# Kernel tuning notes

Measured on AMD Instinct MI355X. Metric: run time of the kernel, lower is better.

## Reference

```python
import jax, jax.numpy as jnp
import numpy as np

N, E, DIM, EDIM, H, T = 30000, 300000, 64, 16, 3, 6


def setup_inputs() -> dict:
    key = jax.random.key(0)
    ks = jax.random.split(key, 20)
    s = 0.1
    inp = {
        'x': jax.random.normal(ks[0], (N, DIM), jnp.float32),
        'edge_index': jax.random.randint(ks[1], (2, E), 0, N, jnp.int64),
        'edge_attr': jax.random.normal(ks[2], (E, EDIM), jnp.float32),
        # EdgeGATConv params (heads=3, out per head = DIM, concat=False -> head mean)
        'Wg': jax.random.normal(ks[3], (DIM, H * DIM), jnp.float32) * s,
        'bg': jnp.zeros((DIM,), jnp.float32),
        'a_src': jax.random.normal(ks[4], (H, DIM), jnp.float32) * s,
        'a_dst': jax.random.normal(ks[5], (H, DIM), jnp.float32) * s,
        'We': jax.random.normal(ks[6], (EDIM, H * DIM), jnp.float32) * s,
        'a_edge': jax.random.normal(ks[7], (H, DIM), jnp.float32) * s,
        # GRU (1 layer), torch gate order: r, z, n
        'Wih': jax.random.normal(ks[8], (3 * DIM, DIM), jnp.float32) * s,
        'Whh': jax.random.normal(ks[9], (3 * DIM, DIM), jnp.float32) * s,
        'bih': jnp.zeros((3 * DIM,), jnp.float32),
        'bhh': jnp.zeros((3 * DIM,), jnp.float32),
        # NodeLevelBatchNorm per time step
        'gamma': jnp.ones((T, DIM), jnp.float32),
        'beta': jnp.zeros((T, DIM), jnp.float32),
        # final linear: dim*(T+1) -> dim
        'Wlin': jax.random.normal(ks[10], (DIM * (T + 1), DIM), jnp.float32) * s,
        'blin': jnp.zeros((DIM,), jnp.float32),
    }
    return inp


def _edge_gat(x, edge_index, edge_attr, Wg, bg, a_src, a_dst, We, a_edge):
    n = x.shape[0]
    xw = (x @ Wg).reshape(n, H, DIM)                 # [N,H,C]
    ew = (edge_attr @ We).reshape(-1, H, DIM)        # [E,H,C]
    src, dst = edge_index[0], edge_index[1]
    logits = ((xw[src] * a_src).sum(-1)
              + (xw[dst] * a_dst).sum(-1)
              + (ew * a_edge).sum(-1))               # [E,H]
    logits = jax.nn.leaky_relu(logits, 0.2)
    # segment softmax over incoming edges per destination node
    amax = jax.ops.segment_max(logits, dst, num_segments=n)
    amax = jnp.where(jnp.isfinite(amax), amax, 0.0)
    ex = jnp.exp(logits - amax[dst])
    denom = jax.ops.segment_sum(ex, dst, num_segments=n)
    att = ex / (denom[dst] + 1e-16)                  # [E,H]
    agg = jax.ops.segment_sum(xw[src] * att[..., None], dst, num_segments=n)  # [N,H,C]
    return agg.mean(axis=1) + bg                     # concat=False: head mean


def _gru_step(m, h, Wih, Whh, bih, bhh):
    gi = m @ Wih.T + bih
    gh = h @ Whh.T + bhh
    ir, iz, inn = jnp.split(gi, 3, axis=-1)
    hr, hz, hn = jnp.split(gh, 3, axis=-1)
    r = jax.nn.sigmoid(ir + hr)
    z = jax.nn.sigmoid(iz + hz)
    nn_ = jnp.tanh(inn + r * hn)
    return (1.0 - z) * nn_ + z * h


def _node_bn(x, gamma, beta, eps=1e-5):
    mu = x.mean(axis=0)
    var = ((x - mu) ** 2).mean(axis=0)
    return (x - mu) * jax.lax.rsqrt(var + eps) * gamma + beta


def reference(x, edge_index, edge_attr, Wg, bg, a_src, a_dst, We, a_edge,
              Wih, Whh, bih, bhh, gamma, beta, Wlin, blin):
    h = x
    feats = [x]
    for i in range(T):
        m = jax.nn.celu(_edge_gat(x, edge_index, edge_attr, Wg, bg, a_src, a_dst, We, a_edge))
        h = _gru_step(m, h, Wih, Whh, bih, bhh)
        x = _node_bn(h, gamma[i], beta[i])
        feats.append(x)
    return jnp.concatenate(feats, axis=-1) @ Wlin + blin
```

## Files before the change

kernel.cpp:

```cpp
#include <hip/hip_runtime.h>
#include <math.h>

constexpr int N_ = 30000;
constexpr int E_ = 300000;
constexpr int SCB = (N_ + 255) / 256;
constexpr int GB_ = (N_ + 63) / 64;

using f32x4  = __attribute__((ext_vector_type(4))) float;
using bf16x8 = __attribute__((ext_vector_type(8))) short;

__device__ __forceinline__ float4 ldg4(const float* p){ return *reinterpret_cast<const float4*>(p); }

__device__ __forceinline__ unsigned short f2bf(float f){
  union { float f; unsigned int u; } v; v.f = f;
  unsigned int r = v.u + 0x7FFFu + ((v.u >> 16) & 1u);
  return (unsigned short)(r >> 16);
}
__device__ __forceinline__ float bf2f(unsigned short b){
  union { unsigned int u; float f; } v; v.u = ((unsigned int)b) << 16;
  return v.f;
}
__device__ __forceinline__ float sigmoidf_(float x){ return 1.0f/(1.0f + __expf(-x)); }


__global__ void k_wfrag(const float* __restrict__ Wg, const float* __restrict__ Wih,
                        const float* __restrict__ Whh, const float* __restrict__ Wlin,
                        const float* __restrict__ We, const float* __restrict__ a_edge,
                        unsigned short* __restrict__ fG, unsigned short* __restrict__ fI,
                        unsigned short* __restrict__ fH, unsigned short* __restrict__ fL,
                        float* __restrict__ P, int* __restrict__ deg){
  if (blockIdx.x >= 257){
    int i = (blockIdx.x - 257)*256 + threadIdx.x;
    if (i < N_) deg[i] = 0;
    return;
  }
  if (blockIdx.x == 256){
    int t = threadIdx.x; if (t >= 48) return;
    int j = t / 3, h = t % 3;
    float s = 0.f;
    for (int c = 0; c < 64; ++c) s += We[j*192 + h*64 + c] * a_edge[h*64 + c];
    P[j*3 + h] = s;
    return;
  }
  int id = blockIdx.x*256 + threadIdx.x;
  int lid, KT;
  unsigned short* dst; int mode;
  if (id < 12288)      { lid = id;         KT = 2;  dst = fG; mode = 0; }
  else if (id < 24576) { lid = id - 12288; KT = 2;  dst = fI; mode = 1; }
  else if (id < 36864) { lid = id - 24576; KT = 2;  dst = fH; mode = 2; }
  else                 { lid = id - 36864; KT = 14; dst = fL; mode = 3; }
  int j = lid & 7, l = (lid >> 3) & 63, rest = lid >> 9;
  int kt = rest % KT, nt = rest / KT;
  int k = kt*32 + (l>>4)*8 + j;
  int n = nt*16 + (l&15);
  float v;
  if (mode == 0)      v = Wg[k*192 + n];
  else if (mode == 1) v = Wih[n*64 + k];
  else if (mode == 2) v = Whh[n*64 + k];
  else                v = Wlin[k*64 + n];
  dst[lid] = f2bf(v);
}

__global__ void k_hist(const int* __restrict__ ei, int* __restrict__ deg){
  int e = blockIdx.x*256 + threadIdx.x;
  if (e < E_) atomicAdd(&deg[ei[E_ + e]], 1);
}

__global__ void k_scanA(const int* __restrict__ deg, int* __restrict__ partial){
  int i = blockIdx.x*256 + threadIdx.x;
  int v = (i < N_) ? deg[i] : 0;
  #pragma unroll
  for (int off = 1; off < 64; off <<= 1) v += __shfl_xor(v, off);
  __shared__ int ws[4];
  if ((threadIdx.x & 63) == 0) ws[threadIdx.x >> 6] = v;
  __syncthreads();
  if (threadIdx.x == 0) partial[blockIdx.x] = ws[0] + ws[1] + ws[2] + ws[3];
}

__global__ void k_scanB(int* __restrict__ partial, int* __restrict__ row_ptr){
  __shared__ int s[128];
  int t = threadIdx.x;
  int v = (t < SCB) ? partial[t] : 0;
  s[t] = v; __syncthreads();
  for (int off = 1; off < 128; off <<= 1){
    int u = (t >= off) ? s[t-off] : 0;
    __syncthreads();
    s[t] += u;
    __syncthreads();
  }
  if (t < SCB) partial[t] = s[t] - v;
  if (t == 0) row_ptr[N_] = E_;
}

__global__ void k_scanC(const int* __restrict__ deg, const int* __restrict__ partial,
                        int* __restrict__ row_ptr, int* __restrict__ cursor){
  __shared__ int s[256];
  int t = threadIdx.x, i = blockIdx.x*256 + t;
  int v = (i < N_) ? deg[i] : 0;
  s[t] = v; __syncthreads();
  for (int off = 1; off < 256; off <<= 1){
    int u = (t >= off) ? s[t-off] : 0;
    __syncthreads();
    s[t] += u;
    __syncthreads();
  }
  int ex = s[t] - v + partial[blockIdx.x];
  if (i < N_){ row_ptr[i] = ex; cursor[i] = ex; }
}

__global__ void k_scatter(const int* __restrict__ ei, const float* __restrict__ edge_attr,
                          const float* __restrict__ P,
                          int* __restrict__ cursor, int* __restrict__ src_s,
                          int* __restrict__ dst_s, float* __restrict__ el_s){
  __shared__ float sP[48];
  int t = threadIdx.x;
  if (t < 48) sP[t] = P[t];
  __syncthreads();
  int e = blockIdx.x*256 + t;
  if (e >= E_) return;
  const float* ea = edge_attr + (size_t)e*16;
  float v[16];
  #pragma unroll
  for (int q = 0; q < 4; ++q){
    float4 f = ldg4(ea + q*4);
    v[q*4+0]=f.x; v[q*4+1]=f.y; v[q*4+2]=f.z; v[q*4+3]=f.w;
  }
  float l0=0.f,l1=0.f,l2=0.f;
  #pragma unroll
  for (int j = 0; j < 16; ++j){
    l0 += v[j]*sP[j*3+0]; l1 += v[j]*sP[j*3+1]; l2 += v[j]*sP[j*3+2];
  }
  int d = ei[E_ + e];
  int p = atomicAdd(&cursor[d], 1);
  src_s[p] = ei[e];
  dst_s[p] = d;
  el_s[p*3+0] = l0; el_s[p*3+1] = l1; el_s[p*3+2] = l2;
}


__global__ __launch_bounds__(256) void k_xw(
    const float* __restrict__ hsrc,
    const float* __restrict__ bn_stats,
    const float* __restrict__ gamma, const float* __restrict__ beta,
    int gidx, int bn,
    const unsigned short* __restrict__ fG,
    const float* __restrict__ a_src, const float* __restrict__ a_dst,
    unsigned short* __restrict__ xw,
    float* __restrict__ asrc, float* __restrict__ adst,
    unsigned short* __restrict__ fr)
{
  __shared__ short sAf[8*64*8];
  __shared__ unsigned short sXW[64*196];
  __shared__ float sSc[64], sSh[64];
  const int t = threadIdx.x;
  const int row0 = blockIdx.x * 64;
  if (t < 64){
    float sc = 1.f, sh = 0.f;
    if (bn){
      float mu  = bn_stats[t] * (1.0f/30000.0f);
      float var = bn_stats[64+t] * (1.0f/30000.0f) - mu*mu;
      float rs = rsqrtf(var + 1e-5f);
      sc = gamma[gidx*64 + t] * rs;
      sh = beta[gidx*64 + t] - mu*sc;
    }
    sSc[t] = sc; sSh[t] = sh;
  }
  __syncthreads();
  {
    const int lr = t >> 4, k4 = (t & 15) * 4;
    const float sc0=sSc[k4],sc1=sSc[k4+1],sc2=sSc[k4+2],sc3=sSc[k4+3];
    const float sh0=sSh[k4],sh1=sSh[k4+1],sh2=sSh[k4+2],sh3=sSh[k4+3];
    const int kt = k4 >> 5, lanew = lr + (((k4>>3)&3)<<4), j0 = k4 & 7;
    #pragma unroll
    for (int i = 0; i < 4; ++i){
      int r = lr + i*16, gr = row0 + r;
      float4 v = make_float4(0.f,0.f,0.f,0.f);
      if (gr < N_){
        v = ldg4(hsrc + (size_t)gr*64 + k4);
        v.x = fmaf(v.x, sc0, sh0); v.y = fmaf(v.y, sc1, sh1);
        v.z = fmaf(v.z, sc2, sh2); v.w = fmaf(v.w, sc3, sh3);
      }
      ushort4 pk; pk.x=f2bf(v.x); pk.y=f2bf(v.y); pk.z=f2bf(v.z); pk.w=f2bf(v.w);
      *reinterpret_cast<ushort4*>(&sAf[((i*2+kt)*64 + lanew)*8 + j0]) = pk;
    }
  }
  __syncthreads();
  {
    bf16x8 v0 = *reinterpret_cast<bf16x8*>(&sAf[t*8]);
    bf16x8 v1 = *reinterpret_cast<bf16x8*>(&sAf[2048 + t*8]);
    bf16x8* g = reinterpret_cast<bf16x8*>(fr + (size_t)blockIdx.x*4096);
    g[t] = v0; g[256 + t] = v1;
  }
  const int w = t >> 6, l = t & 63, q = l >> 4, b = l & 15;
  f32x4 acc[12];
  #pragma unroll
  for (int nt = 0; nt < 12; ++nt) acc[nt] = (f32x4){0.f,0.f,0.f,0.f};
  bf16x8 a0 = *reinterpret_cast<bf16x8*>(&sAf[((w*2+0)*64 + l)*8]);
  bf16x8 a1 = *reinterpret_cast<bf16x8*>(&sAf[((w*2+1)*64 + l)*8]);
  #pragma unroll
  for (int nt = 0; nt < 12; ++nt){
    bf16x8 b0 = *reinterpret_cast<const bf16x8*>(fG + (size_t)((nt*2+0)*64 + l)*8);
    bf16x8 b1 = *reinterpret_cast<const bf16x8*>(fG + (size_t)((nt*2+1)*64 + l)*8);
    acc[nt] = __builtin_amdgcn_mfma_f32_16x16x32_bf16(a0, b0, acc[nt], 0, 0, 0);
    acc[nt] = __builtin_amdgcn_mfma_f32_16x16x32_bf16(a1, b1, acc[nt], 0, 0, 0);
  }
  float asl[3][4], adl[3][4];
  #pragma unroll
  for (int h = 0; h < 3; ++h)
    #pragma unroll
    for (int u = 0; u < 4; ++u){
      asl[h][u] = a_src[h*64 + u*16 + b];
      adl[h][u] = a_dst[h*64 + u*16 + b];
    }
  #pragma unroll
  for (int r = 0; r < 4; ++r){
    int gr = row0 + w*16 + q*4 + r;
    #pragma unroll
    for (int h = 0; h < 3; ++h){
      float s = 0.f, d = 0.f;
      #pragma unroll
      for (int u = 0; u < 4; ++u){
        s = fmaf(acc[4*h+u][r], asl[h][u], s);
        d = fmaf(acc[4*h+u][r], adl[h][u], d);
      }
      s += __shfl_xor(s,1); s += __shfl_xor(s,2); s += __shfl_xor(s,4); s += __shfl_xor(s,8);
      d += __shfl_xor(d,1); d += __shfl_xor(d,2); d += __shfl_xor(d,4); d += __shfl_xor(d,8);
      if (b == h && gr < N_){ asrc[gr*3+h] = s; adst[gr*3+h] = d; }
    }
  }
  #pragma unroll
  for (int nt = 0; nt < 12; ++nt){
    int col = nt*16 + b;
    #pragma unroll
    for (int r = 0; r < 4; ++r)
      sXW[(w*16 + q*4 + r)*196 + col] = f2bf(acc[nt][r]);
  }
  __syncthreads();
  #pragma unroll
  for (int i = 0; i < 16; ++i){
    int id = i*256 + t;
    int row = id >> 6, c2 = id & 63, gr = row0 + row;
    if (gr < N_){
      ushort4 pv;
      pv.x = sXW[row*196 + c2];
      pv.y = sXW[row*196 + 64 + c2];
      pv.z = sXW[row*196 + 128 + c2];
      pv.w = 0;
      *reinterpret_cast<ushort4*>(xw + ((size_t)gr << 8) + (c2 << 2)) = pv;
    }
  }
}

__global__ void k_att(const int* __restrict__ src_s, const int* __restrict__ dst_s,
                      const float* __restrict__ el_s,
                      const float* __restrict__ asrc, const float* __restrict__ adst,
                      float* __restrict__ att_s){
  int p = blockIdx.x*256 + threadIdx.x;
  if (p >= E_) return;
  int s = src_s[p], d = dst_s[p];
  #pragma unroll
  for (int h = 0; h < 3; ++h){
    float l = asrc[s*3+h] + adst[d*3+h] + el_s[p*3+h];
    l = l > 0.f ? l : 0.2f*l;
    att_s[p*3+h] = __expf(l);
  }
}

__global__ __launch_bounds__(256) void k_agg(
    const int* __restrict__ row_ptr, const int* __restrict__ src_s,
    const float* __restrict__ att_s,
    const unsigned short* __restrict__ xw,
    const float* __restrict__ bg,
    float* __restrict__ mbuf, float* __restrict__ bn_stats)
{
  if (blockIdx.x == 0 && threadIdx.x < 128) bn_stats[threadIdx.x] = 0.f;
  int n = blockIdx.x*4 + (threadIdx.x >> 6);
  int c = threadIdx.x & 63;
  if (n >= N_) return;
  int p0 = row_ptr[n], p1 = row_ptr[n+1];
  float d0 = 0.f, d1 = 0.f, d2 = 0.f;
  float a0 = 0.f, a1 = 0.f, a2 = 0.f;
  int p = p0;
  for (; p + 4 <= p1; p += 4){
    int sA = src_s[p], sB = src_s[p+1], sC = src_s[p+2], sD = src_s[p+3];
    ushort4 gA = *reinterpret_cast<const ushort4*>(xw + ((size_t)sA << 8) + (c << 2));
    ushort4 gB = *reinterpret_cast<const ushort4*>(xw + ((size_t)sB << 8) + (c << 2));
    ushort4 gC = *reinterpret_cast<const ushort4*>(xw + ((size_t)sC << 8) + (c << 2));
    ushort4 gD = *reinterpret_cast<const ushort4*>(xw + ((size_t)sD << 8) + (c << 2));
    float wA0 = att_s[p*3+0],  wA1 = att_s[p*3+1],  wA2 = att_s[p*3+2];
    float wB0 = att_s[p*3+3],  wB1 = att_s[p*3+4],  wB2 = att_s[p*3+5];
    float wC0 = att_s[p*3+6],  wC1 = att_s[p*3+7],  wC2 = att_s[p*3+8];
    float wD0 = att_s[p*3+9],  wD1 = att_s[p*3+10], wD2 = att_s[p*3+11];
    d0 += (wA0 + wB0) + (wC0 + wD0);
    d1 += (wA1 + wB1) + (wC1 + wD1);
    d2 += (wA2 + wB2) + (wC2 + wD2);
    a0 = fmaf(wA0, bf2f(gA.x), a0); a1 = fmaf(wA1, bf2f(gA.y), a1); a2 = fmaf(wA2, bf2f(gA.z), a2);
    a0 = fmaf(wB0, bf2f(gB.x), a0); a1 = fmaf(wB1, bf2f(gB.y), a1); a2 = fmaf(wB2, bf2f(gB.z), a2);
    a0 = fmaf(wC0, bf2f(gC.x), a0); a1 = fmaf(wC1, bf2f(gC.y), a1); a2 = fmaf(wC2, bf2f(gC.z), a2);
    a0 = fmaf(wD0, bf2f(gD.x), a0); a1 = fmaf(wD1, bf2f(gD.y), a1); a2 = fmaf(wD2, bf2f(gD.z), a2);
  }
  for (; p < p1; ++p){
    int s = src_s[p];
    ushort4 g = *reinterpret_cast<const ushort4*>(xw + ((size_t)s << 8) + (c << 2));
    float w0 = att_s[p*3+0], w1 = att_s[p*3+1], w2 = att_s[p*3+2];
    d0 += w0; d1 += w1; d2 += w2;
    a0 = fmaf(w0, bf2f(g.x), a0);
    a1 = fmaf(w1, bf2f(g.y), a1);
    a2 = fmaf(w2, bf2f(g.z), a2);
  }
  float mp = (a0/(d0+1e-16f) + a1/(d1+1e-16f) + a2/(d2+1e-16f)) * (1.0f/3.0f) + bg[c];
  mbuf[(size_t)n*64 + c] = mp > 0.f ? mp : (__expf(mp) - 1.0f);
}

__global__ __launch_bounds__(256) void k_gru(
    const float* __restrict__ mbuf, const float* __restrict__ hsrc,
    float* __restrict__ hbuf,
    const unsigned short* __restrict__ fI, const unsigned short* __restrict__ fH,
    const float* __restrict__ bih, const float* __restrict__ bhh,
    float* __restrict__ bn_stats)
{
  __shared__ short sMf[8*64*8];
  __shared__ short sHf[8*64*8];
  __shared__ float sH[64][68];
  __shared__ float sStat[128];
  const int t = threadIdx.x;
  const int row0 = blockIdx.x * 64;
  if (t < 128) sStat[t] = 0.f;
  {
    const int lr = t >> 4, k4 = (t & 15) * 4;
    const int kt = k4 >> 5, lanew = lr + (((k4>>3)&3)<<4), j0 = k4 & 7;
    #pragma unroll
    for (int i = 0; i < 4; ++i){
      int r = lr + i*16, gr = row0 + r;
      float4 vm = make_float4(0.f,0.f,0.f,0.f), vh = vm;
      if (gr < N_){ vm = ldg4(mbuf + (size_t)gr*64 + k4); vh = ldg4(hsrc + (size_t)gr*64 + k4); }
      ushort4 pm; pm.x=f2bf(vm.x); pm.y=f2bf(vm.y); pm.z=f2bf(vm.z); pm.w=f2bf(vm.w);
      ushort4 ph; ph.x=f2bf(vh.x); ph.y=f2bf(vh.y); ph.z=f2bf(vh.z); ph.w=f2bf(vh.w);
      *reinterpret_cast<ushort4*>(&sMf[((i*2+kt)*64 + lanew)*8 + j0]) = pm;
      *reinterpret_cast<ushort4*>(&sHf[((i*2+kt)*64 + lanew)*8 + j0]) = ph;
      sH[r][k4+0]=vh.x; sH[r][k4+1]=vh.y; sH[r][k4+2]=vh.z; sH[r][k4+3]=vh.w;
    }
  }
  __syncthreads();
  const int w = t >> 6, l = t & 63, q = l >> 4, b = l & 15;
  f32x4 aI[12], aH[12];
  #pragma unroll
  for (int nt = 0; nt < 12; ++nt){ aI[nt] = (f32x4){0.f,0.f,0.f,0.f}; aH[nt] = (f32x4){0.f,0.f,0.f,0.f}; }
  bf16x8 am0 = *reinterpret_cast<bf16x8*>(&sMf[((w*2+0)*64 + l)*8]);
  bf16x8 am1 = *reinterpret_cast<bf16x8*>(&sMf[((w*2+1)*64 + l)*8]);
  bf16x8 ah0 = *reinterpret_cast<bf16x8*>(&sHf[((w*2+0)*64 + l)*8]);
  bf16x8 ah1 = *reinterpret_cast<bf16x8*>(&sHf[((w*2+1)*64 + l)*8]);
  #pragma unroll
  for (int nt = 0; nt < 12; ++nt){
    bf16x8 bI0 = *reinterpret_cast<const bf16x8*>(fI + (size_t)((nt*2+0)*64 + l)*8);
    bf16x8 bI1 = *reinterpret_cast<const bf16x8*>(fI + (size_t)((nt*2+1)*64 + l)*8);
    bf16x8 bH0 = *reinterpret_cast<const bf16x8*>(fH + (size_t)((nt*2+0)*64 + l)*8);
    bf16x8 bH1 = *reinterpret_cast<const bf16x8*>(fH + (size_t)((nt*2+1)*64 + l)*8);
    aI[nt] = __builtin_amdgcn_mfma_f32_16x16x32_bf16(am0, bI0, aI[nt], 0, 0, 0);
    aI[nt] = __builtin_amdgcn_mfma_f32_16x16x32_bf16(am1, bI1, aI[nt], 0, 0, 0);
    aH[nt] = __builtin_amdgcn_mfma_f32_16x16x32_bf16(ah0, bH0, aH[nt], 0, 0, 0);
    aH[nt] = __builtin_amdgcn_mfma_f32_16x16x32_bf16(ah1, bH1, aH[nt], 0, 0, 0);
  }
  float s1[4] = {0.f,0.f,0.f,0.f}, s2[4] = {0.f,0.f,0.f,0.f};
  #pragma unroll
  for (int tt = 0; tt < 4; ++tt){
    int c = tt*16 + b;
    float bir = bih[c], biz = bih[64+c], bin = bih[128+c];
    float bhr = bhh[c], bhz = bhh[64+c], bhn = bhh[128+c];
    #pragma unroll
    for (int r = 0; r < 4; ++r){
      int row = w*16 + q*4 + r, gr = row0 + row;
      float rg = sigmoidf_(aI[tt][r]   + bir + aH[tt][r]   + bhr);
      float zg = sigmoidf_(aI[tt+4][r] + biz + aH[tt+4][r] + bhz);
      float ng = tanhf(aI[tt+8][r] + bin + rg*(aH[tt+8][r] + bhn));
      float ho = sH[row][c];
      float hv = (1.f - zg)*ng + zg*ho;
      if (gr < N_){
        hbuf[(size_t)gr*64 + c] = hv;
        s1[tt] += hv; s2[tt] += hv*hv;
      }
    }
  }
  #pragma unroll
  for (int tt = 0; tt < 4; ++tt){
    float v = s1[tt];
    v += __shfl_xor(v, 16); v += __shfl_xor(v, 32);
    float u = s2[tt];
    u += __shfl_xor(u, 16); u += __shfl_xor(u, 32);
    if (q == 0){
      atomicAdd(&sStat[tt*16 + b], v);
      atomicAdd(&sStat[64 + tt*16 + b], u);
    }
  }
  __syncthreads();
  if (t < 128) atomicAdd(&bn_stats[t], sStat[t]);
}

__global__ __launch_bounds__(256) void k_final(
    const unsigned short* __restrict__ ff, const float* __restrict__ hbuf,
    const float* __restrict__ bn_stats,
    const float* __restrict__ gamma, const float* __restrict__ beta,
    const unsigned short* __restrict__ fL, const float* __restrict__ blin,
    float* __restrict__ out)
{
  __shared__ short sAf[8*64*8];
  __shared__ float sSc[64], sSh[64];
  const int t = threadIdx.x;
  const int row0 = blockIdx.x * 64;
  if (t < 64){
    float mu  = bn_stats[t] * (1.0f/30000.0f);
    float var = bn_stats[64+t] * (1.0f/30000.0f) - mu*mu;
    float rs = rsqrtf(var + 1e-5f);
    float sc = gamma[5*64 + t] * rs;
    sSc[t] = sc;
    sSh[t] = beta[5*64 + t] - mu*sc;
  }
  __syncthreads();
  const int w = t >> 6, l = t & 63, q = l >> 4, b = l & 15;
  const int lr = t >> 4, k4 = (t & 15) * 4;
  const int kt = k4 >> 5, lanew = lr + (((k4>>3)&3)<<4), j0 = k4 & 7;
  {
    #pragma unroll
    for (int i = 0; i < 4; ++i){
      int r = lr + i*16, gr = row0 + r;
      float4 v = make_float4(0.f,0.f,0.f,0.f);
      if (gr < N_){
        v = ldg4(hbuf + (size_t)gr*64 + k4);
        v.x = fmaf(v.x, sSc[k4+0], sSh[k4+0]);
        v.y = fmaf(v.y, sSc[k4+1], sSh[k4+1]);
        v.z = fmaf(v.z, sSc[k4+2], sSh[k4+2]);
        v.w = fmaf(v.w, sSc[k4+3], sSh[k4+3]);
      }
      ushort4 pk; pk.x=f2bf(v.x); pk.y=f2bf(v.y); pk.z=f2bf(v.z); pk.w=f2bf(v.w);
      *reinterpret_cast<ushort4*>(&sAf[((i*2+kt)*64 + lanew)*8 + j0]) = pk;
    }
  }
  __syncthreads();
  f32x4 acc[4];
  #pragma unroll
  for (int nt = 0; nt < 4; ++nt) acc[nt] = (f32x4){0.f,0.f,0.f,0.f};
  const unsigned short* fb = ff + (size_t)blockIdx.x*4096;
  #pragma unroll
  for (int kc = 0; kc < 6; ++kc){
    const unsigned short* fs = fb + (size_t)kc*GB_*4096;
    bf16x8 a0 = *reinterpret_cast<const bf16x8*>(fs + (w*2+0)*512 + l*8);
    bf16x8 a1 = *reinterpret_cast<const bf16x8*>(fs + (w*2+1)*512 + l*8);
    #pragma unroll
    for (int nt = 0; nt < 4; ++nt){
      bf16x8 b0 = *reinterpret_cast<const bf16x8*>(fL + (size_t)((nt*14 + kc*2+0)*64 + l)*8);
      bf16x8 b1 = *reinterpret_cast<const bf16x8*>(fL + (size_t)((nt*14 + kc*2+1)*64 + l)*8);
      acc[nt] = __builtin_amdgcn_mfma_f32_16x16x32_bf16(a0, b0, acc[nt], 0, 0, 0);
      acc[nt] = __builtin_amdgcn_mfma_f32_16x16x32_bf16(a1, b1, acc[nt], 0, 0, 0);
    }
  }
  {
    bf16x8 a0 = *reinterpret_cast<bf16x8*>(&sAf[((w*2+0)*64 + l)*8]);
    bf16x8 a1 = *reinterpret_cast<bf16x8*>(&sAf[((w*2+1)*64 + l)*8]);
    #pragma unroll
    for (int nt = 0; nt < 4; ++nt){
      bf16x8 b0 = *reinterpret_cast<const bf16x8*>(fL + (size_t)((nt*14 + 12)*64 + l)*8);
      bf16x8 b1 = *reinterpret_cast<const bf16x8*>(fL + (size_t)((nt*14 + 13)*64 + l)*8);
      acc[nt] = __builtin_amdgcn_mfma_f32_16x16x32_bf16(a0, b0, acc[nt], 0, 0, 0);
      acc[nt] = __builtin_amdgcn_mfma_f32_16x16x32_bf16(a1, b1, acc[nt], 0, 0, 0);
    }
  }
  #pragma unroll
  for (int nt = 0; nt < 4; ++nt){
    int col = nt*16 + b;
    float bl = blin[col];
    #pragma unroll
    for (int r = 0; r < 4; ++r){
      int gr = row0 + w*16 + q*4 + r;
      if (gr < N_) out[(size_t)gr*64 + col] = acc[nt][r] + bl;
    }
  }
}


extern "C" void kernel_launch(void* const* d_in, const int* in_sizes, int n_in,
                              void* d_out, int out_size, void* d_ws, size_t ws_size,
                              hipStream_t stream) {
  const float* x        = (const float*)d_in[0];
  const int*   ei       = (const int*)  d_in[1];
  const float* edge_attr= (const float*)d_in[2];
  const float* Wg       = (const float*)d_in[3];
  const float* bg       = (const float*)d_in[4];
  const float* a_src    = (const float*)d_in[5];
  const float* a_dst    = (const float*)d_in[6];
  const float* We       = (const float*)d_in[7];
  const float* a_edge   = (const float*)d_in[8];
  const float* Wih      = (const float*)d_in[9];
  const float* Whh      = (const float*)d_in[10];
  const float* bih      = (const float*)d_in[11];
  const float* bhh      = (const float*)d_in[12];
  const float* gamma    = (const float*)d_in[13];
  const float* beta     = (const float*)d_in[14];
  const float* Wlin     = (const float*)d_in[15];
  const float* blin     = (const float*)d_in[16];
  float* out = (float*)d_out;

  char* w = (char*)d_ws;
  auto alloc = [&](size_t bytes) -> void* {
    void* p = (void*)w;
    w += (bytes + 255) & ~(size_t)255;
    return p;
  };
  int*   row_ptr = (int*)  alloc((size_t)(N_+1)*4);
  int*   deg     = (int*)  alloc((size_t)N_*4);
  int*   cursor  = (int*)  alloc((size_t)N_*4);
  int*   partial = (int*)  alloc(128*4);
  int*   src_s   = (int*)  alloc((size_t)E_*4);
  int*   dst_s   = (int*)  alloc((size_t)E_*4);
  float* el_s    = (float*)alloc((size_t)E_*3*4);
  float* att_s   = (float*)alloc((size_t)E_*3*4);
  float* Pw      = (float*)alloc(48*4);
  unsigned short* fG = (unsigned short*)alloc(12288*2);
  unsigned short* fI = (unsigned short*)alloc(12288*2);
  unsigned short* fH = (unsigned short*)alloc(12288*2);
  unsigned short* fL = (unsigned short*)alloc(28672*2);
  unsigned short* xw = (unsigned short*)alloc((size_t)N_*256*2);
  unsigned short* ffrag = (unsigned short*)alloc((size_t)6*GB_*4096*2);
  float* asrc    = (float*)alloc((size_t)N_*3*4);
  float* adst    = (float*)alloc((size_t)N_*3*4);
  float* mbuf    = (float*)alloc((size_t)N_*64*4);
  float* hbuf    = (float*)alloc((size_t)N_*64*4);
  float* bn_stats= (float*)alloc(128*4);

  const int EB = (E_ + 255)/256;

  k_wfrag  <<<257 + SCB, 256, 0, stream>>>(Wg, Wih, Whh, Wlin, We, a_edge,
                                           fG, fI, fH, fL, Pw, deg);
  k_hist   <<<EB, 256, 0, stream>>>(ei, deg);
  k_scanA  <<<SCB, 256, 0, stream>>>(deg, partial);
  k_scanB  <<<1, 128, 0, stream>>>(partial, row_ptr);
  k_scanC  <<<SCB, 256, 0, stream>>>(deg, partial, row_ptr, cursor);
  k_scatter<<<EB, 256, 0, stream>>>(ei, edge_attr, Pw, cursor, src_s, dst_s, el_s);

  for (int step = 0; step < 6; ++step){
    const float* hsrc = (step == 0) ? x : hbuf;
    k_xw <<<GB_, 256, 0, stream>>>(hsrc, bn_stats, gamma, beta,
                                   step-1, step > 0 ? 1 : 0,
                                   fG, a_src, a_dst, xw, asrc, adst,
                                   ffrag + (size_t)step*GB_*4096);
    k_att<<<EB, 256, 0, stream>>>(src_s, dst_s, el_s, asrc, adst, att_s);
    k_agg<<<(N_+3)/4, 256, 0, stream>>>(row_ptr, src_s, att_s, xw, bg, mbuf, bn_stats);
    k_gru<<<GB_, 256, 0, stream>>>(mbuf, hsrc, hbuf, fI, fH, bih, bhh, bn_stats);
  }
  k_final<<<GB_, 256, 0, stream>>>(ffrag, hbuf, bn_stats, gamma, beta, fL, blin, out);
}
```

Measured before the change: 559.0 us.

## Fuse attention, aggregation and GRU into one kernel per step

Removes the separate attention and aggregation kernels. Edge logits are now recomputed inside the aggregation loop, and the aggregated message is written straight into the GRU's shared-memory bf16 fragments instead of a global mbuf. The dst_s, att_s and mbuf buffers go away, and BN stats become per-step slices zeroed once at setup. The cost is that aggregation now runs at 64-row-block granularity with one wave per row sequentially, which lowers parallelism for the gather phase, and the unroll drops from 4 to 2.

```diff
diff --git a/kernel.cpp b/kernel.cpp
--- a/kernel.cpp
+++ b/kernel.cpp
@@ -28,7 +28,12 @@
                         const float* __restrict__ We, const float* __restrict__ a_edge,
                         unsigned short* __restrict__ fG, unsigned short* __restrict__ fI,
                         unsigned short* __restrict__ fH, unsigned short* __restrict__ fL,
-                        float* __restrict__ P, int* __restrict__ deg){
+                        float* __restrict__ P, int* __restrict__ deg,
+                        float* __restrict__ bn_stats){
+  if (blockIdx.x == 257 + SCB){
+    for (int k = threadIdx.x; k < 768; k += 256) bn_stats[k] = 0.f;
+    return;
+  }
   if (blockIdx.x >= 257){
     int i = (blockIdx.x - 257)*256 + threadIdx.x;
     if (i < N_) deg[i] = 0;
@@ -111,7 +116,7 @@
 __global__ void k_scatter(const int* __restrict__ ei, const float* __restrict__ edge_attr,
                           const float* __restrict__ P,
                           int* __restrict__ cursor, int* __restrict__ src_s,
-                          int* __restrict__ dst_s, float* __restrict__ el_s){
+                          float* __restrict__ el_s){
   __shared__ float sP[48];
   int t = threadIdx.x;
   if (t < 48) sP[t] = P[t];
@@ -133,7 +138,6 @@
   int d = ei[E_ + e];
   int p = atomicAdd(&cursor[d], 1);
   src_s[p] = ei[e];
-  dst_s[p] = d;
   el_s[p*3+0] = l0; el_s[p*3+1] = l1; el_s[p*3+2] = l2;
 }
 
@@ -251,70 +255,12 @@
   }
 }
 
-__global__ void k_att(const int* __restrict__ src_s, const int* __restrict__ dst_s,
-                      const float* __restrict__ el_s,
-                      const float* __restrict__ asrc, const float* __restrict__ adst,
-                      float* __restrict__ att_s){
-  int p = blockIdx.x*256 + threadIdx.x;
-  if (p >= E_) return;
-  int s = src_s[p], d = dst_s[p];
-  #pragma unroll
-  for (int h = 0; h < 3; ++h){
-    float l = asrc[s*3+h] + adst[d*3+h] + el_s[p*3+h];
-    l = l > 0.f ? l : 0.2f*l;
-    att_s[p*3+h] = __expf(l);
-  }
-}
-
-__global__ __launch_bounds__(256) void k_agg(
+__global__ __launch_bounds__(256) void k_aggru(
     const int* __restrict__ row_ptr, const int* __restrict__ src_s,
-    const float* __restrict__ att_s,
-    const unsigned short* __restrict__ xw,
-    const float* __restrict__ bg,
-    float* __restrict__ mbuf, float* __restrict__ bn_stats)
-{
-  if (blockIdx.x == 0 && threadIdx.x < 128) bn_stats[threadIdx.x] = 0.f;
-  int n = blockIdx.x*4 + (threadIdx.x >> 6);
-  int c = threadIdx.x & 63;
-  if (n >= N_) return;
-  int p0 = row_ptr[n], p1 = row_ptr[n+1];
-  float d0 = 0.f, d1 = 0.f, d2 = 0.f;
-  float a0 = 0.f, a1 = 0.f, a2 = 0.f;
-  int p = p0;
-  for (; p + 4 <= p1; p += 4){
-    int sA = src_s[p], sB = src_s[p+1], sC = src_s[p+2], sD = src_s[p+3];
-    ushort4 gA = *reinterpret_cast<const ushort4*>(xw + ((size_t)sA << 8) + (c << 2));
-    ushort4 gB = *reinterpret_cast<const ushort4*>(xw + ((size_t)sB << 8) + (c << 2));
-    ushort4 gC = *reinterpret_cast<const ushort4*>(xw + ((size_t)sC << 8) + (c << 2));
-    ushort4 gD = *reinterpret_cast<const ushort4*>(xw + ((size_t)sD << 8) + (c << 2));
-    float wA0 = att_s[p*3+0],  wA1 = att_s[p*3+1],  wA2 = att_s[p*3+2];
-    float wB0 = att_s[p*3+3],  wB1 = att_s[p*3+4],  wB2 = att_s[p*3+5];
-    float wC0 = att_s[p*3+6],  wC1 = att_s[p*3+7],  wC2 = att_s[p*3+8];
-    float wD0 = att_s[p*3+9],  wD1 = att_s[p*3+10], wD2 = att_s[p*3+11];
-    d0 += (wA0 + wB0) + (wC0 + wD0);
-    d1 += (wA1 + wB1) + (wC1 + wD1);
-    d2 += (wA2 + wB2) + (wC2 + wD2);
-    a0 = fmaf(wA0, bf2f(gA.x), a0); a1 = fmaf(wA1, bf2f(gA.y), a1); a2 = fmaf(wA2, bf2f(gA.z), a2);
-    a0 = fmaf(wB0, bf2f(gB.x), a0); a1 = fmaf(wB1, bf2f(gB.y), a1); a2 = fmaf(wB2, bf2f(gB.z), a2);
-    a0 = fmaf(wC0, bf2f(gC.x), a0); a1 = fmaf(wC1, bf2f(gC.y), a1); a2 = fmaf(wC2, bf2f(gC.z), a2);
-    a0 = fmaf(wD0, bf2f(gD.x), a0); a1 = fmaf(wD1, bf2f(gD.y), a1); a2 = fmaf(wD2, bf2f(gD.z), a2);
-  }
-  for (; p < p1; ++p){
-    int s = src_s[p];
-    ushort4 g = *reinterpret_cast<const ushort4*>(xw + ((size_t)s << 8) + (c << 2));
-    float w0 = att_s[p*3+0], w1 = att_s[p*3+1], w2 = att_s[p*3+2];
-    d0 += w0; d1 += w1; d2 += w2;
-    a0 = fmaf(w0, bf2f(g.x), a0);
-    a1 = fmaf(w1, bf2f(g.y), a1);
-    a2 = fmaf(w2, bf2f(g.z), a2);
-  }
-  float mp = (a0/(d0+1e-16f) + a1/(d1+1e-16f) + a2/(d2+1e-16f)) * (1.0f/3.0f) + bg[c];
-  mbuf[(size_t)n*64 + c] = mp > 0.f ? mp : (__expf(mp) - 1.0f);
-}
-
-__global__ __launch_bounds__(256) void k_gru(
-    const float* __restrict__ mbuf, const float* __restrict__ hsrc,
-    float* __restrict__ hbuf,
+    const float* __restrict__ el_s,
+    const float* __restrict__ asrc, const float* __restrict__ adst,
+    const unsigned short* __restrict__ xw, const float* __restrict__ bg,
+    const float* __restrict__ hsrc, float* __restrict__ hbuf,
     const unsigned short* __restrict__ fI, const unsigned short* __restrict__ fH,
     const float* __restrict__ bih, const float* __restrict__ bhh,
     float* __restrict__ bn_stats)
@@ -332,17 +278,62 @@
     #pragma unroll
     for (int i = 0; i < 4; ++i){
       int r = lr + i*16, gr = row0 + r;
-      float4 vm = make_float4(0.f,0.f,0.f,0.f), vh = vm;
-      if (gr < N_){ vm = ldg4(mbuf + (size_t)gr*64 + k4); vh = ldg4(hsrc + (size_t)gr*64 + k4); }
-      ushort4 pm; pm.x=f2bf(vm.x); pm.y=f2bf(vm.y); pm.z=f2bf(vm.z); pm.w=f2bf(vm.w);
+      float4 vh = make_float4(0.f,0.f,0.f,0.f);
+      if (gr < N_) vh = ldg4(hsrc + (size_t)gr*64 + k4);
       ushort4 ph; ph.x=f2bf(vh.x); ph.y=f2bf(vh.y); ph.z=f2bf(vh.z); ph.w=f2bf(vh.w);
-      *reinterpret_cast<ushort4*>(&sMf[((i*2+kt)*64 + lanew)*8 + j0]) = pm;
       *reinterpret_cast<ushort4*>(&sHf[((i*2+kt)*64 + lanew)*8 + j0]) = ph;
       sH[r][k4+0]=vh.x; sH[r][k4+1]=vh.y; sH[r][k4+2]=vh.z; sH[r][k4+3]=vh.w;
     }
   }
-  __syncthreads();
-  const int w = t >> 6, l = t & 63, q = l >> 4, b = l & 15;
+  const int w = t >> 6, c = t & 63;
+  for (int it = 0; it < 16; ++it){
+    int r = w*16 + it, n = row0 + r;
+    int fidx = (((r>>4)*2 + (c>>5))*64 + (r&15) + (((c>>3)&3)<<4))*8 + (c&7);
+    unsigned short mv = 0;
+    if (n < N_){
+      int p0 = row_ptr[n], p1 = row_ptr[n+1];
+      float ad0 = adst[n*3+0], ad1 = adst[n*3+1], ad2 = adst[n*3+2];
+      float d0=0.f,d1=0.f,d2=0.f,a0=0.f,a1=0.f,a2=0.f;
+      int p = p0;
+      for (; p + 2 <= p1; p += 2){
+        int sA = src_s[p], sB = src_s[p+1];
+        ushort4 gA = *reinterpret_cast<const ushort4*>(xw + ((size_t)sA << 8) + (c << 2));
+        ushort4 gB = *reinterpret_cast<const ushort4*>(xw + ((size_t)sB << 8) + (c << 2));
+        float lA0 = asrc[sA*3+0] + ad0 + el_s[p*3+0];
+        float lA1 = asrc[sA*3+1] + ad1 + el_s[p*3+1];
+        float lA2 = asrc[sA*3+2] + ad2 + el_s[p*3+2];
+        float lB0 = asrc[sB*3+0] + ad0 + el_s[p*3+3];
+        float lB1 = asrc[sB*3+1] + ad1 + el_s[p*3+4];
+        float lB2 = asrc[sB*3+2] + ad2 + el_s[p*3+5];
+        lA0 = lA0>0.f?lA0:0.2f*lA0; lA1 = lA1>0.f?lA1:0.2f*lA1; lA2 = lA2>0.f?lA2:0.2f*lA2;
+        lB0 = lB0>0.f?lB0:0.2f*lB0; lB1 = lB1>0.f?lB1:0.2f*lB1; lB2 = lB2>0.f?lB2:0.2f*lB2;
+        float wA0 = __expf(lA0), wA1 = __expf(lA1), wA2 = __expf(lA2);
+        float wB0 = __expf(lB0), wB1 = __expf(lB1), wB2 = __expf(lB2);
+        d0 += wA0 + wB0; d1 += wA1 + wB1; d2 += wA2 + wB2;
+        a0 = fmaf(wA0, bf2f(gA.x), a0); a1 = fmaf(wA1, bf2f(gA.y), a1); a2 = fmaf(wA2, bf2f(gA.z), a2);
+        a0 = fmaf(wB0, bf2f(gB.x), a0); a1 = fmaf(wB1, bf2f(gB.y), a1); a2 = fmaf(wB2, bf2f(gB.z), a2);
+      }
+      if (p < p1){
+        int s = src_s[p];
+        ushort4 g = *reinterpret_cast<const ushort4*>(xw + ((size_t)s << 8) + (c << 2));
+        float l0 = asrc[s*3+0] + ad0 + el_s[p*3+0];
+        float l1 = asrc[s*3+1] + ad1 + el_s[p*3+1];
+        float l2 = asrc[s*3+2] + ad2 + el_s[p*3+2];
+        l0 = l0>0.f?l0:0.2f*l0; l1 = l1>0.f?l1:0.2f*l1; l2 = l2>0.f?l2:0.2f*l2;
+        float w0 = __expf(l0), w1 = __expf(l1), w2 = __expf(l2);
+        d0 += w0; d1 += w1; d2 += w2;
+        a0 = fmaf(w0, bf2f(g.x), a0);
+        a1 = fmaf(w1, bf2f(g.y), a1);
+        a2 = fmaf(w2, bf2f(g.z), a2);
+      }
+      float mp = (a0/(d0+1e-16f) + a1/(d1+1e-16f) + a2/(d2+1e-16f)) * (1.0f/3.0f) + bg[c];
+      mp = mp > 0.f ? mp : (__expf(mp) - 1.0f);
+      mv = f2bf(mp);
+    }
+    sMf[fidx] = (short)mv;
+  }
+  __syncthreads();
+  const int l = t & 63, q = l >> 4, b = l & 15;
   f32x4 aI[12], aH[12];
   #pragma unroll
   for (int nt = 0; nt < 12; ++nt){ aI[nt] = (f32x4){0.f,0.f,0.f,0.f}; aH[nt] = (f32x4){0.f,0.f,0.f,0.f}; }
@@ -364,19 +355,19 @@
   float s1[4] = {0.f,0.f,0.f,0.f}, s2[4] = {0.f,0.f,0.f,0.f};
   #pragma unroll
   for (int tt = 0; tt < 4; ++tt){
-    int c = tt*16 + b;
-    float bir = bih[c], biz = bih[64+c], bin = bih[128+c];
-    float bhr = bhh[c], bhz = bhh[64+c], bhn = bhh[128+c];
+    int cc = tt*16 + b;
+    float bir = bih[cc], biz = bih[64+cc], bin = bih[128+cc];
+    float bhr = bhh[cc], bhz = bhh[64+cc], bhn = bhh[128+cc];
     #pragma unroll
     for (int r = 0; r < 4; ++r){
       int row = w*16 + q*4 + r, gr = row0 + row;
       float rg = sigmoidf_(aI[tt][r]   + bir + aH[tt][r]   + bhr);
       float zg = sigmoidf_(aI[tt+4][r] + biz + aH[tt+4][r] + bhz);
       float ng = tanhf(aI[tt+8][r] + bin + rg*(aH[tt+8][r] + bhn));
-      float ho = sH[row][c];
+      float ho = sH[row][cc];
       float hv = (1.f - zg)*ng + zg*ho;
       if (gr < N_){
-        hbuf[(size_t)gr*64 + c] = hv;
+        hbuf[(size_t)gr*64 + cc] = hv;
         s1[tt] += hv; s2[tt] += hv*hv;
       }
     }
@@ -510,9 +501,7 @@
   int*   cursor  = (int*)  alloc((size_t)N_*4);
   int*   partial = (int*)  alloc(128*4);
   int*   src_s   = (int*)  alloc((size_t)E_*4);
-  int*   dst_s   = (int*)  alloc((size_t)E_*4);
   float* el_s    = (float*)alloc((size_t)E_*3*4);
-  float* att_s   = (float*)alloc((size_t)E_*3*4);
   float* Pw      = (float*)alloc(48*4);
   unsigned short* fG = (unsigned short*)alloc(12288*2);
   unsigned short* fI = (unsigned short*)alloc(12288*2);
@@ -522,29 +511,30 @@
   unsigned short* ffrag = (unsigned short*)alloc((size_t)6*GB_*4096*2);
   float* asrc    = (float*)alloc((size_t)N_*3*4);
   float* adst    = (float*)alloc((size_t)N_*3*4);
-  float* mbuf    = (float*)alloc((size_t)N_*64*4);
   float* hbuf    = (float*)alloc((size_t)N_*64*4);
-  float* bn_stats= (float*)alloc(128*4);
+  float* bn_stats= (float*)alloc(768*4);
 
   const int EB = (E_ + 255)/256;
 
-  k_wfrag  <<<257 + SCB, 256, 0, stream>>>(Wg, Wih, Whh, Wlin, We, a_edge,
-                                           fG, fI, fH, fL, Pw, deg);
+  k_wfrag  <<<258 + SCB, 256, 0, stream>>>(Wg, Wih, Whh, Wlin, We, a_edge,
+                                           fG, fI, fH, fL, Pw, deg, bn_stats);
   k_hist   <<<EB, 256, 0, stream>>>(ei, deg);
   k_scanA  <<<SCB, 256, 0, stream>>>(deg, partial);
   k_scanB  <<<1, 128, 0, stream>>>(partial, row_ptr);
   k_scanC  <<<SCB, 256, 0, stream>>>(deg, partial, row_ptr, cursor);
-  k_scatter<<<EB, 256, 0, stream>>>(ei, edge_attr, Pw, cursor, src_s, dst_s, el_s);
+  k_scatter<<<EB, 256, 0, stream>>>(ei, edge_attr, Pw, cursor, src_s, el_s);
 
   for (int step = 0; step < 6; ++step){
     const float* hsrc = (step == 0) ? x : hbuf;
-    k_xw <<<GB_, 256, 0, stream>>>(hsrc, bn_stats, gamma, beta,
-                                   step-1, step > 0 ? 1 : 0,
+    k_xw <<<GB_, 256, 0, stream>>>(hsrc,
+                                   bn_stats + (size_t)(step > 0 ? step-1 : 0)*128,
+                                   gamma, beta, step-1, step > 0 ? 1 : 0,
                                    fG, a_src, a_dst, xw, asrc, adst,
                                    ffrag + (size_t)step*GB_*4096);
-    k_att<<<EB, 256, 0, stream>>>(src_s, dst_s, el_s, asrc, adst, att_s);
-    k_agg<<<(N_+3)/4, 256, 0, stream>>>(row_ptr, src_s, att_s, xw, bg, mbuf, bn_stats);
-    k_gru<<<GB_, 256, 0, stream>>>(mbuf, hsrc, hbuf, fI, fH, bih, bhh, bn_stats);
-  }
-  k_final<<<GB_, 256, 0, stream>>>(ffrag, hbuf, bn_stats, gamma, beta, fL, blin, out);
-}
+    k_aggru<<<GB_, 256, 0, stream>>>(row_ptr, src_s, el_s, asrc, adst, xw, bg,
+                                     hsrc, hbuf, fI, fH, bih, bhh,
+                                     bn_stats + (size_t)step*128);
+  }
+  k_final<<<GB_, 256, 0, stream>>>(ffrag, hbuf, bn_stats + 5*128,
+                                   gamma, beta, fL, blin, out);
+}
```

Measured after the change: 777.1 us. 1.39x slower.
